# Optimization experiments

Measured on AMD Instinct MI355X. Metric: run time of the kernel, lower is better.

The kernel has to match this reference:

```python
import jax, jax.numpy as jnp
import numpy as np
from jax import lax

NEG = -1e30  # safe -inf surrogate (avoids inf-inf NaNs under vjp)


def setup_inputs() -> dict:
    key = jax.random.key(0)
    k1, k2, k3, k4 = jax.random.split(key, 4)
    B, T, U, V = 8, 128, 64, 1024
    acts = jax.random.normal(k1, (B, T, U + 1, V), dtype=jnp.float32)
    # labels in [1, V): blank (0) never appears in target sequences
    labels = jax.random.randint(k2, (B, U), 1, V, dtype=jnp.int32)
    act_lens = jax.random.randint(k3, (B,), T // 2, T + 1, dtype=jnp.int32)
    label_lens = jax.random.randint(k4, (B,), U // 2, U + 1, dtype=jnp.int32)
    return {"acts": acts, "labels": labels, "act_lens": act_lens, "label_lens": label_lens}


def _rnnt_costs(acts, labels, act_lens, label_lens, blank=0):
    """Per-example negative log-likelihood of the RNNT alignment lattice.
    acts: (B, T, U+1, V) logits (warp_rnnt applies log_softmax internally).
    """
    B, T, U1, V = acts.shape
    U = U1 - 1
    lp = jax.nn.log_softmax(acts, axis=-1)
    lp_blank = lp[..., blank]                                        # (B, T, U+1)
    lab = jnp.broadcast_to(labels[:, None, :, None], (B, T, U, 1))
    lp_label = jnp.take_along_axis(lp[:, :, :U, :], lab, axis=3)[..., 0]  # (B, T, U)
    # mask label emissions beyond each example's label length
    umask = jnp.arange(U)[None, :] < label_lens[:, None]             # (B, U)
    lp_label = jnp.where(umask[:, None, :], lp_label, NEG)

    def compute_row(fb, lt):
        # fb: (B, U+1) alpha[t-1, u] + lp_blank[t-1, u] (the "from below" term)
        # lt: (B, U)   label log-probs at time t
        # new[u] = logaddexp(fb[u], new[u-1] + lt[u-1])  -- sequential in u
        def u_step(carry, x):
            fb_u, lt_u = x
            new = jnp.logaddexp(fb_u, carry + lt_u)
            return new, new
        _, rest = lax.scan(u_step, fb[:, 0], (fb[:, 1:].T, lt.T))    # (U, B)
        return jnp.concatenate([fb[:, 0:1], rest.T], axis=1)         # (B, U+1)

    # t = 0 row: alpha[0,0] = 0; only label transitions along u
    fb0 = jnp.concatenate([jnp.zeros((B, 1), acts.dtype), jnp.full((B, U), NEG, acts.dtype)], axis=1)
    row0 = compute_row(fb0, lp_label[:, 0, :])

    def t_step(prev_row, x):
        lpb_prev, lt = x
        row = compute_row(prev_row + lpb_prev, lt)
        return row, row

    xs = (jnp.moveaxis(lp_blank[:, :-1, :], 0, 1),   # (T-1, B, U+1)
          jnp.moveaxis(lp_label[:, 1:, :], 0, 1))    # (T-1, B, U)
    _, rows = lax.scan(t_step, row0, xs)             # (T-1, B, U+1)
    alphas = jnp.concatenate([row0[None], rows], axis=0)  # (T, B, U+1)

    b = jnp.arange(B)
    tl = act_lens - 1
    final = alphas[tl, b, label_lens] + lp_blank[b, tl, label_lens]
    return -final                                     # (B,)


def reference(acts, labels, act_lens, label_lens):
    # matches torch module defaults: size_average=False, blank_label=0
    costs = _rnnt_costs(acts, labels, act_lens, label_lens, blank=0)
    return jnp.sum(costs).reshape(1)
```

## Files before the change

### kernel.cpp

```cpp
#include <hip/hip_runtime.h>

#define LN2F 0.6931471805599453f

#define B_   8
#define T_   128
#define U_   64
#define U1_  65
#define V_   1024
#define CW_  132
#define CB_  (T_*CW_)
#define ROWS_ (B_*T_*U1_)
#define NWAVES_ 8192
#define K1_BLOCKS_ 2048

typedef float f32x4 __attribute__((ext_vector_type(4)));

__device__ __forceinline__ float shr1_f32(float x) {
  return __int_as_float(__builtin_amdgcn_update_dpp(
      0, __float_as_int(x), 0x138, 0xf, 0xf, true));
}

__device__ __forceinline__ int wave_max_bexp(float a, float i0) {
  int e  = (int)((__float_as_uint(a)  >> 23) & 0xffu);
  int e2 = (int)((__float_as_uint(i0) >> 23) & 0xffu);
  e = max(e, e2);
  int t;
  t = __builtin_amdgcn_update_dpp(e, e, 0x111, 0xf, 0xf, false); e = max(e, t);
  t = __builtin_amdgcn_update_dpp(e, e, 0x112, 0xf, 0xf, false); e = max(e, t);
  t = __builtin_amdgcn_update_dpp(e, e, 0x114, 0xf, 0xf, false); e = max(e, t);
  t = __builtin_amdgcn_update_dpp(e, e, 0x118, 0xf, 0xf, false); e = max(e, t);
  t = __builtin_amdgcn_update_dpp(e, e, 0x142, 0xf, 0xf, false); e = max(e, t);
  t = __builtin_amdgcn_update_dpp(e, e, 0x143, 0xf, 0xf, false); e = max(e, t);
  return __builtin_amdgcn_readlane(e, 63);
}

__global__ __launch_bounds__(256) void k1_linsoftmax(
    const float* __restrict__ acts, const int* __restrict__ labels,
    const int* __restrict__ label_lens,
    float* __restrict__ cglob, float* __restrict__ pb0, int* __restrict__ cnt) {
  const int lane = threadIdx.x & 63;
  const int wid  = blockIdx.x * 4 + (threadIdx.x >> 6);
  if (wid == 0 && lane == 0) *cnt = 0;

  for (int row = wid; row < ROWS_; row += NWAVES_) {
    const int b   = row / (T_ * U1_);
    const int rem = row - b * (T_ * U1_);
    const int t   = rem / U1_;
    const int u   = rem - t * U1_;
    const float* __restrict__ p = acts + (size_t)row * V_;

    int ll_ = 0; float labv = 0.0f;
    if (lane == 0 && u < U_) {
      ll_  = label_lens[b];
      labv = p[labels[b * U_ + u]];
    }

    f32x4 v0 = *(const f32x4*)(p +   0 + lane * 4);
    f32x4 v1 = *(const f32x4*)(p + 256 + lane * 4);
    f32x4 v2 = *(const f32x4*)(p + 512 + lane * 4);
    f32x4 v3 = *(const f32x4*)(p + 768 + lane * 4);

    float m = fmaxf(fmaxf(fmaxf(v0.x, v0.y), fmaxf(v0.z, v0.w)),
              fmaxf(fmaxf(fmaxf(v1.x, v1.y), fmaxf(v1.z, v1.w)),
              fmaxf(fmaxf(fmaxf(v2.x, v2.y), fmaxf(v2.z, v2.w)),
                    fmaxf(fmaxf(v3.x, v3.y), fmaxf(v3.z, v3.w)))));
    #pragma unroll
    for (int o = 32; o; o >>= 1) m = fmaxf(m, __shfl_xor(m, o, 64));

    float e00 = __expf(v0.x - m);
    float s = e00          + __expf(v0.y - m) + __expf(v0.z - m) + __expf(v0.w - m)
            + __expf(v1.x - m) + __expf(v1.y - m) + __expf(v1.z - m) + __expf(v1.w - m)
            + __expf(v2.x - m) + __expf(v2.y - m) + __expf(v2.z - m) + __expf(v2.w - m)
            + __expf(v3.x - m) + __expf(v3.y - m) + __expf(v3.z - m) + __expf(v3.w - m);
    #pragma unroll
    for (int o = 32; o; o >>= 1) s += __shfl_xor(s, o, 64);

    if (lane == 0) {
      float rs = 1.0f / s;
      float pb = e00 * rs;
      int   rb = (b * T_ + t) * CW_;
      if (u == 0) pb0[b * T_ + t] = pb;
      else        cglob[rb + 2 * u - 1] = pb;
      if (u < U_) {
        float elab = __expf(labv - m);
        cglob[rb + 2 * u] = (u < ll_) ? (elab * rs) : 0.0f;
      }
    }
  }
}

__global__ __launch_bounds__(256) void k2_alpha(
    const float* __restrict__ cglob, const float* __restrict__ pb0,
    const int* __restrict__ act_lens, const int* __restrict__ label_lens,
    float* __restrict__ costs, int* __restrict__ cnt, float* __restrict__ out) {
  __shared__ float c_s[CB_];
  __shared__ float col0_s[256];
  const int b = blockIdx.x;

  {
    const f32x4* src = (const f32x4*)(cglob + (size_t)b * CB_);
    f32x4* dst = (f32x4*)c_s;
    for (int i = threadIdx.x; i < CB_ / 4; i += 256) dst[i] = src[i];
    for (int i = threadIdx.x; i < T_; i += 256) col0_s[i] = pb0[b * T_ + i];
  }
  __syncthreads();
  for (int i = threadIdx.x; i < T_; i += 256) col0_s[128 + i] = c_s[i * CW_];
  __syncthreads();
  if (threadIdx.x >= 64) return;

  const int l  = (int)threadIdx.x;
  const int tl = act_lens[b] - 1;
  const int ll = label_lens[b];
  const int u  = l + 1;
  const int dcap = (u == ll) ? (tl + ll) : 0x7fffffff;

  const float2* __restrict__ c2 = (const float2*)c_s;
  const int pairbase = u - 1;

  float a = 0.0f;
  float i0 = (l == 0) ? 1.0f : 0.0f;
  float fin = 0.0f;
  int   S = 0, vE = 0, Ecap = 0;
  int   tm = -u;
  int   rc = -1;

  float2 pA[8], pB[8];
  float  b0A[8], l0A[8], b0B[8], l0B[8];

#define LOADB(P, B0, L0) do {                                            \
    _Pragma("unroll")                                                    \
    for (int j = 0; j < 8; ++j) {                                        \
      tm += 1;                                                           \
      int r = min(max(tm, 0), T_ - 1);                                   \
      (P)[j] = c2[r * 66 + pairbase];                                    \
      rc = min(rc + 1, T_ - 1);                                          \
      (B0)[j] = col0_s[rc];                                              \
      (L0)[j] = col0_s[rc + 128];                                        \
    }                                                                    \
  } while (0)

#define RENORM() do {                                                    \
    int eS = wave_max_bexp(a, i0);                                       \
    int sh = 167 - eS;                 \
    S += sh;                                                             \
    float sc = ldexpf(1.0f, sh);                                         \
    a *= sc; i0 *= sc;                                                   \
    vE = S;                                                              \
  } while (0)

#define COMPUTE(P, B0, L0, DB) do {                                      \
    _Pragma("unroll")                                                    \
    for (int j = 0; j < 8; ++j) {                                        \
      const int dc = (DB) + j;                                           \
      float shin = shr1_f32(a);                                          \
      float inj  = i0 * (L0)[j];                                         \
      a = fmaf(a, pbc, fmaf(shin, (P)[j].x, inj));                       \
      if (dc == dcap) { fin = a; Ecap = vE; }                            \
      i0 *= (B0)[j];                                                     \
      pbc = (P)[j].y;                                                    \
    }                                                                    \
  } while (0)

  LOADB(pA, b0A, l0A);
  float pbc = c_s[2 * u - 1];

  #pragma unroll 1
  for (int kb = 0; kb < 12; ++kb) {
    LOADB(pB, b0B, l0B);
    if (kb > 0) RENORM();
    COMPUTE(pA, b0A, l0A, 16 * kb + 1);
    if (kb < 11) LOADB(pA, b0A, l0A);
    RENORM();
    COMPUTE(pB, b0B, l0B, 16 * kb + 9);
  }
#undef LOADB
#undef RENORM
#undef COMPUTE

  if (u == ll) {
    float pblast = c_s[tl * CW_ + 2 * ll - 1];
    float lg = __log2f(fin) - (float)Ecap + __log2f(pblast);
    costs[b] = -lg * LN2F;
  }

  __threadfence();
  if (l == 0) {
    int old = atomicAdd(cnt, 1);
    if (old == B_ - 1) {
      __threadfence();
      volatile const float* vc = costs;
      float s = 0.0f;
      #pragma unroll
      for (int i = 0; i < B_; ++i) s += vc[i];
      out[0] = s;
    }
  }
}

extern "C" void kernel_launch(void* const* d_in, const int* in_sizes, int n_in,
                              void* d_out, int out_size, void* d_ws, size_t ws_size,
                              hipStream_t stream) {
  const float* acts       = (const float*)d_in[0];
  const int*   labels     = (const int*)d_in[1];
  const int*   act_lens   = (const int*)d_in[2];
  const int*   label_lens = (const int*)d_in[3];

  float* cglob = (float*)d_ws;
  float* pb0   = cglob + (size_t)B_ * CB_;
  float* costs = pb0 + B_ * T_;
  int*   cnt   = (int*)(costs + B_);

  k1_linsoftmax<<<K1_BLOCKS_, 256, 0, stream>>>(acts, labels, label_lens, cglob, pb0, cnt);
  k2_alpha<<<B_, 256, 0, stream>>>(cglob, pb0, act_lens, label_lens, costs, cnt, (float*)d_out);
}
```

Before: 63.25 us.

## Store lattice coefficients diagonal-major and stream them from global in alpha kernel

The softmax kernel now writes blank and label probabilities into a diagonal-packed float2 layout, so each lane of the alpha wavefront reads one contiguous entry per anti-diagonal. The alpha kernel no longer stages a per-batch block into shared memory and launches only 64 threads. It loads 16 diagonals at a time straight from global or L2. This removes the shared-memory staging and the two barriers before the serial recurrence. In exchange, every step now depends on global load latency and on the prefetch hiding it, and the pack buffer is never zero-initialised, so unwritten or padding slots may hold stale workspace data.

```diff
diff --git a/kernel.cpp b/kernel.cpp
--- a/kernel.cpp
+++ b/kernel.cpp
@@ -7,9 +7,11 @@
 #define U_   64
 #define U1_  65
 #define V_   1024
-#define CW_  132
-#define CB_  (T_*CW_)
 #define ROWS_ (B_*T_*U1_)
+#define NDIAG_ 224
+#define DS_    66
+#define PACKB_ (NDIAG_*DS_)
+#define COL0N_ 224
 #define NWAVES_ 8192
 #define K1_BLOCKS_ 2048
 
@@ -37,7 +39,7 @@
 __global__ __launch_bounds__(256) void k1_linsoftmax(
     const float* __restrict__ acts, const int* __restrict__ labels,
     const int* __restrict__ label_lens,
-    float* __restrict__ cglob, float* __restrict__ pb0, int* __restrict__ cnt) {
+    float2* __restrict__ pack, float2* __restrict__ col0, int* __restrict__ cnt) {
   const int lane = threadIdx.x & 63;
   const int wid  = blockIdx.x * 4 + (threadIdx.x >> 6);
   if (wid == 0 && lane == 0) *cnt = 0;
@@ -78,107 +80,103 @@
     if (lane == 0) {
       float rs = 1.0f / s;
       float pb = e00 * rs;
-      int   rb = (b * T_ + t) * CW_;
-      if (u == 0) pb0[b * T_ + t] = pb;
-      else        cglob[rb + 2 * u - 1] = pb;
-      if (u < U_) {
-        float elab = __expf(labv - m);
-        cglob[rb + 2 * u] = (u < ll_) ? (elab * rs) : 0.0f;
+      float2* pk = pack + (size_t)b * PACKB_;
+      if (u == 0) {
+        float pl0 = __expf(labv - m) * rs;
+        col0[b * COL0N_ + (t + 1)] = make_float2(pb, pl0);
+        pk[(size_t)(t + 1) * DS_ + 1].x = pl0;
+      } else {
+        pk[(size_t)(t + u) * DS_ + u].y = pb;
+        if (u < U_) {
+          float plv = (u < ll_) ? (__expf(labv - m) * rs) : 0.0f;
+          pk[(size_t)(t + u + 1) * DS_ + (u + 1)].x = plv;
+        }
       }
     }
   }
 }
 
-__global__ __launch_bounds__(256) void k2_alpha(
-    const float* __restrict__ cglob, const float* __restrict__ pb0,
+__global__ __launch_bounds__(64) void k2_alpha(
+    const float2* __restrict__ pack, const float2* __restrict__ col0,
     const int* __restrict__ act_lens, const int* __restrict__ label_lens,
     float* __restrict__ costs, int* __restrict__ cnt, float* __restrict__ out) {
-  __shared__ float c_s[CB_];
-  __shared__ float col0_s[256];
-  const int b = blockIdx.x;
-
-  {
-    const f32x4* src = (const f32x4*)(cglob + (size_t)b * CB_);
-    f32x4* dst = (f32x4*)c_s;
-    for (int i = threadIdx.x; i < CB_ / 4; i += 256) dst[i] = src[i];
-    for (int i = threadIdx.x; i < T_; i += 256) col0_s[i] = pb0[b * T_ + i];
-  }
-  __syncthreads();
-  for (int i = threadIdx.x; i < T_; i += 256) col0_s[128 + i] = c_s[i * CW_];
-  __syncthreads();
-  if (threadIdx.x >= 64) return;
-
+  const int b  = (int)blockIdx.x;
   const int l  = (int)threadIdx.x;
   const int tl = act_lens[b] - 1;
   const int ll = label_lens[b];
   const int u  = l + 1;
-  const int dcap = (u == ll) ? (tl + ll) : 0x7fffffff;
-
-  const float2* __restrict__ c2 = (const float2*)c_s;
-  const int pairbase = u - 1;
+  const int tcap = (u == ll) ? tl : 0x7fffffff;
+
+  const float2* __restrict__ pku = pack + (size_t)b * PACKB_ + u;
+  const float2* __restrict__ c0  = col0 + (size_t)b * COL0N_;
 
   float a = 0.0f;
   float i0 = (l == 0) ? 1.0f : 0.0f;
-  float fin = 0.0f;
-  int   S = 0, vE = 0, Ecap = 0;
-  int   tm = -u;
-  int   rc = -1;
-
-  float2 pA[8], pB[8];
-  float  b0A[8], l0A[8], b0B[8], l0B[8];
-
-#define LOADB(P, B0, L0) do {                                            \
+  float fin = 0.0f, pbc = 0.0f;
+  int   S = 0, Ecap = 0;
+  int   t_ = -u;
+
+  float2 pA[16], pB[16], cA[16], cB[16];
+
+#define LOADP(P, C, DB) do {                                             \
+    const float2* q_ = pku + (size_t)(DB) * DS_;                         \
     _Pragma("unroll")                                                    \
-    for (int j = 0; j < 8; ++j) {                                        \
-      tm += 1;                                                           \
-      int r = min(max(tm, 0), T_ - 1);                                   \
-      (P)[j] = c2[r * 66 + pairbase];                                    \
-      rc = min(rc + 1, T_ - 1);                                          \
-      (B0)[j] = col0_s[rc];                                              \
-      (L0)[j] = col0_s[rc + 128];                                        \
+    for (int j = 0; j < 16; ++j) (P)[j] = q_[(size_t)j * DS_];           \
+    _Pragma("unroll")                                                    \
+    for (int j = 0; j < 16; ++j) {                                       \
+      float2 cv_ = c0[(DB) + j];                                         \
+      bool ok_ = ((DB) + j) <= T_;                  \
+      (C)[j].x = ok_ ? cv_.x : 0.0f;                                     \
+      (C)[j].y = ok_ ? cv_.y : 0.0f;                                     \
     }                                                                    \
   } while (0)
 
 #define RENORM() do {                                                    \
-    int eS = wave_max_bexp(a, i0);                                       \
-    int sh = 167 - eS;                 \
-    S += sh;                                                             \
-    float sc = ldexpf(1.0f, sh);                                         \
-    a *= sc; i0 *= sc;                                                   \
-    vE = S;                                                              \
+    int eS_ = wave_max_bexp(a, i0);                                      \
+    int sh_ = min(167 - eS_, 126);     \
+    S += sh_;                                                            \
+    float sc_ = ldexpf(1.0f, sh_);                                       \
+    a *= sc_; i0 *= sc_;                                                 \
   } while (0)
 
-#define COMPUTE(P, B0, L0, DB) do {                                      \
+#define COMPUTE8(P, C, JO) do {                                          \
     _Pragma("unroll")                                                    \
-    for (int j = 0; j < 8; ++j) {                                        \
-      const int dc = (DB) + j;                                           \
+    for (int jj = 0; jj < 8; ++jj) {                                     \
+      const int j = (JO) + jj;                                           \
+      t_ += 1;                                                           \
       float shin = shr1_f32(a);                                          \
-      float inj  = i0 * (L0)[j];                                         \
-      a = fmaf(a, pbc, fmaf(shin, (P)[j].x, inj));                       \
-      if (dc == dcap) { fin = a; Ecap = vE; }                            \
-      i0 *= (B0)[j];                                                     \
+      float inj  = i0 * (C)[j].y;                                        \
+      float anew = fmaf(a, pbc, fmaf(shin, (P)[j].x, inj));              \
+      bool valid = ((unsigned)t_ < (unsigned)T_);                        \
+      a = valid ? anew : 0.0f;                \
+      bool cap = (t_ == tcap);                                           \
+      fin  = cap ? a : fin;                                              \
+      Ecap = cap ? S : Ecap;                                             \
+      i0 *= (C)[j].x;                                                    \
       pbc = (P)[j].y;                                                    \
     }                                                                    \
   } while (0)
 
-  LOADB(pA, b0A, l0A);
-  float pbc = c_s[2 * u - 1];
-
+  LOADP(pA, cA, 1);
   #pragma unroll 1
-  for (int kb = 0; kb < 12; ++kb) {
-    LOADB(pB, b0B, l0B);
-    if (kb > 0) RENORM();
-    COMPUTE(pA, b0A, l0A, 16 * kb + 1);
-    if (kb < 11) LOADB(pA, b0A, l0A);
+  for (int it = 0; it < 12; it += 2) {
+    LOADP(pB, cB, 16 * it + 17);
+    if (it > 0) RENORM();
+    COMPUTE8(pA, cA, 0);
     RENORM();
-    COMPUTE(pB, b0B, l0B, 16 * kb + 9);
-  }
-#undef LOADB
+    COMPUTE8(pA, cA, 8);
+    if (it < 10) LOADP(pA, cA, 16 * it + 33);
+    RENORM();
+    COMPUTE8(pB, cB, 0);
+    RENORM();
+    COMPUTE8(pB, cB, 8);
+  }
+#undef LOADP
 #undef RENORM
-#undef COMPUTE
+#undef COMPUTE8
 
   if (u == ll) {
-    float pblast = c_s[tl * CW_ + 2 * ll - 1];
+    float pblast = pack[(size_t)b * PACKB_ + (size_t)(tl + ll) * DS_ + ll].y;
     float lg = __log2f(fin) - (float)Ecap + __log2f(pblast);
     costs[b] = -lg * LN2F;
   }
@@ -205,11 +203,11 @@
   const int*   act_lens   = (const int*)d_in[2];
   const int*   label_lens = (const int*)d_in[3];
 
-  float* cglob = (float*)d_ws;
-  float* pb0   = cglob + (size_t)B_ * CB_;
-  float* costs = pb0 + B_ * T_;
-  int*   cnt   = (int*)(costs + B_);
-
-  k1_linsoftmax<<<K1_BLOCKS_, 256, 0, stream>>>(acts, labels, label_lens, cglob, pb0, cnt);
-  k2_alpha<<<B_, 256, 0, stream>>>(cglob, pb0, act_lens, label_lens, costs, cnt, (float*)d_out);
-}
+  float2* pack  = (float2*)d_ws;
+  float2* col0  = pack + (size_t)B_ * PACKB_;
+  float*  costs = (float*)(col0 + (size_t)B_ * COL0N_);
+  int*    cnt   = (int*)(costs + B_);
+
+  k1_linsoftmax<<<K1_BLOCKS_, 256, 0, stream>>>(acts, labels, label_lens, pack, col0, cnt);
+  k2_alpha<<<B_, 64, 0, stream>>>(pack, col0, act_lens, label_lens, costs, cnt, (float*)d_out);
+}
```

Result: faster. 61.61 us (-2.6%).
